# Optimization experiments

Hardware: AMD Instinct MI355X
Metric: run time of the kernel (lower is better)

The kernel has to match this reference:

```python
import jax, jax.numpy as jnp
import numpy as np

B = 2048        # graphs per batch
NC = 81         # cells per sudoku
IN_C, HID = 10, 128
N_ACT, N_NUM, N_TECH = 4, 9, 10


def _sudoku_edges():
    idx = np.arange(NC).reshape(9, 9)
    adj = np.zeros((NC, NC), dtype=bool)
    for i in range(9):
        for j in range(9):
            n = idx[i, j]
            adj[n, idx[i, :]] = True
            adj[n, idx[:, j]] = True
            bi, bj = 3 * (i // 3), 3 * (j // 3)
            adj[n, idx[bi:bi + 3, bj:bj + 3].reshape(-1)] = True
            adj[n, n] = False
    src, dst = np.nonzero(adj)  # 1620 directed edges
    return np.stack([src, dst]).astype(np.int32)


def setup_inputs() -> dict:
    key = jax.random.key(0)
    ks = jax.random.split(key, 12)
    N = B * NC
    base = _sudoku_edges()                          # [2, 1620]
    offs = (np.arange(B, dtype=np.int32) * NC)      # [B]
    ei = (base[:, None, :] + offs[None, :, None]).reshape(2, -1)  # [2, B*1620]
    batch = np.repeat(np.arange(B, dtype=np.int32), NC)           # [N]

    def lin(k, fan_in, fan_out):
        s = 1.0 / np.sqrt(fan_in)
        return jax.random.uniform(k, (fan_in, fan_out), jnp.float32, -s, s)

    return {
        "x": jax.random.normal(ks[0], (N, IN_C), jnp.float32),
        "edge_index": jnp.asarray(ei),
        "batch": jnp.asarray(batch),
        "W1": lin(ks[1], IN_C, HID), "b1": jnp.zeros((HID,), jnp.float32),
        "W2": lin(ks[2], HID, HID),  "b2": jnp.zeros((HID,), jnp.float32),
        "Wa": lin(ks[3], HID, N_ACT),  "ba": jnp.zeros((N_ACT,), jnp.float32),
        "Wc": lin(ks[4], HID, NC),     "bc": jnp.zeros((NC,), jnp.float32),
        "Wn": lin(ks[5], HID, N_NUM),  "bn": jnp.zeros((N_NUM,), jnp.float32),
        "Wt": lin(ks[6], HID, N_TECH), "bt": jnp.zeros((N_TECH,), jnp.float32),
    }


def _gcn_conv(x, edge_index, W, b):
    n = x.shape[0]
    loop = jnp.arange(n, dtype=edge_index.dtype)
    src = jnp.concatenate([edge_index[0], loop])
    dst = jnp.concatenate([edge_index[1], loop])
    deg = jax.ops.segment_sum(jnp.ones_like(dst, jnp.float32), dst, num_segments=n)
    dinv = jax.lax.rsqrt(deg)            # deg >= 1 due to self-loops
    norm = dinv[src] * dinv[dst]         # [E+N]
    h = x @ W                            # [N, out]
    msg = h[src] * norm[:, None]         # gather + scale
    return jax.ops.segment_sum(msg, dst, num_segments=n) + b


def reference(x, edge_index, batch, W1, b1, W2, b2, Wa, ba, Wc, bc, Wn, bn, Wt, bt):
    h = jax.nn.relu(_gcn_conv(x, edge_index, W1, b1))
    h = jax.nn.relu(_gcn_conv(h, edge_index, W2, b2))
    # global mean pool over graphs
    sums = jax.ops.segment_sum(h, batch, num_segments=B)
    cnts = jax.ops.segment_sum(jnp.ones((h.shape[0],), h.dtype), batch, num_segments=B)
    pooled = sums / jnp.maximum(cnts, 1.0)[:, None]   # [B, HID]
    return (pooled @ Wa + ba, pooled @ Wc + bc, pooled @ Wn + bn, pooled @ Wt + bt)
```

## Files before the change

### kernel.cpp

```cpp
#include <hip/hip_runtime.h>
#include <hip/hip_bf16.h>

typedef __attribute__((ext_vector_type(8))) short bf16x8;
typedef __attribute__((ext_vector_type(4))) float f32x4;

__device__ __forceinline__ unsigned short f2b(float f) {
    __hip_bfloat16 h = __float2bfloat16(f);
    return __builtin_bit_cast(unsigned short, h);
}
__device__ __forceinline__ float b2f(unsigned short u) {
    unsigned v = ((unsigned)u) << 16;
    return __builtin_bit_cast(float, v);
}
__device__ __forceinline__ float ldf(const void* p, int idx, bool f32) {
    return f32 ? ((const float*)p)[idx] : b2f(((const unsigned short*)p)[idx]);
}
__device__ __forceinline__ unsigned short ldb(const void* p, int idx, bool f32) {
    return f32 ? f2b(((const float*)p)[idx]) : ((const unsigned short*)p)[idx];
}
__device__ __forceinline__ int swz(int row, int col) {
    return row * 128 + (((col >> 3) ^ (row & 7)) << 3) + (col & 7);
}

__device__ __forceinline__ bool sniff_f32(const void* x) {
    const unsigned* p = (const unsigned*)x;
    int wild = 0;
#pragma unroll
    for (int i = 0; i < 16; ++i) {
        unsigned e = (p[i] >> 7) & 0xFF;
        wild += (e != 0 && (e < 0x68 || e > 0x90)) ? 1 : 0;
    }
    return wild > 8;
}

#define WS_B1F    16
#define WS_B2F    528
#define WS_BHF    1040
#define WS_W1R    1536
#define WS_W2R    9728
#define WS_SR     42496
#define WS_WH     60928

__global__ void k_repack(const void* __restrict__ x,
                         const void* __restrict__ W1, const void* __restrict__ b1,
                         const void* __restrict__ W2, const void* __restrict__ b2,
                         const void* __restrict__ Wa, const void* __restrict__ ba,
                         const void* __restrict__ Wc, const void* __restrict__ bc,
                         const void* __restrict__ Wn, const void* __restrict__ bn,
                         const void* __restrict__ Wt, const void* __restrict__ bt,
                         char* __restrict__ ws) {
    const bool f32 = sniff_f32(x);
    int idx = blockIdx.x * blockDim.x + threadIdx.x;
    if (idx < 4096) {
        int f = idx >> 5, k = idx & 31;
        unsigned short v = (k < 10) ? ldb(W1, k * 128 + f, f32) : (unsigned short)0;
        ((unsigned short*)(ws + WS_W1R))[idx] = v;
        return;
    }
    idx -= 4096;
    if (idx < 16384) {
        int f = idx >> 7, k = idx & 127;
        ((unsigned short*)(ws + WS_W2R))[idx] = ldb(W2, k * 128 + f, f32);
        return;
    }
    idx -= 16384;
    if (idx < 9216) {
        int fi = idx >> 9, rem = idx & 511;
        int lane = rem >> 3, j = rem & 7;
        int mi = fi / 3, kc = fi - mi * 3;
        int node = mi * 16 + (lane & 15);
        int cell = kc * 32 + ((lane >> 4) << 3) + j;
        bool adj = false;
        if (node < 81 && cell < 81) {
            int ni = node / 9, nj = node % 9;
            int ci = cell / 9, cj = cell % 9;
            adj = (ni == ci) || (nj == cj) ||
                  ((ni / 3 == ci / 3) && (nj / 3 == cj / 3));
        }
        ((unsigned short*)(ws + WS_SR))[idx] = adj ? (unsigned short)0x3F80 : (unsigned short)0;
        return;
    }
    idx -= 9216;
    if (idx < 13312) {
        int o = idx >> 7, f = idx & 127;
        const void* W; int oo, dim;
        if (o < 4)       { W = Wa; oo = o;      dim = 4;  }
        else if (o < 85) { W = Wc; oo = o - 4;  dim = 81; }
        else if (o < 94) { W = Wn; oo = o - 85; dim = 9;  }
        else             { W = Wt; oo = o - 94; dim = 10; }
        ((float*)(ws + WS_WH))[idx] = ldf(W, f * dim + oo, f32);
        return;
    }
    idx -= 13312;
    if (idx < 360) {
        float v;
        if (idx < 128)      v = ldf(b1, idx, f32);
        else if (idx < 256) v = ldf(b2, idx - 128, f32);
        else {
            int o = idx - 256;
            if (o < 4)       v = ldf(ba, o, f32);
            else if (o < 85) v = ldf(bc, o - 4, f32);
            else if (o < 94) v = ldf(bn, o - 85, f32);
            else             v = ldf(bt, o - 94, f32);
        }
        if (idx < 128)      ((float*)(ws + WS_B1F))[idx] = v;
        else if (idx < 256) ((float*)(ws + WS_B2F))[idx - 128] = v;
        else                ((float*)(ws + WS_BHF))[idx - 256] = v;
    }
}

__global__ __launch_bounds__(256, 4) void sudoku_gnn(
    const void* __restrict__ x, const char* __restrict__ ws,
    void* __restrict__ out, int nB)
{
    __shared__ __attribute__((aligned(16))) unsigned short sA[16384];
    __shared__ __attribute__((aligned(16))) unsigned int   xs[816];
    __shared__ float sPoolPart[256];
    __shared__ float sPool[128];

    const bool f32 = sniff_f32(x);
    const unsigned short* w1r = (const unsigned short*)(ws + WS_W1R);
    const unsigned short* w2r = (const unsigned short*)(ws + WS_W2R);
    const unsigned short* sr  = (const unsigned short*)(ws + WS_SR);
    const float* b1f = (const float*)(ws + WS_B1F);
    const float* b2f = (const float*)(ws + WS_B2F);
    const float* bhf = (const float*)(ws + WS_BHF);
    const float* whf = (const float*)(ws + WS_WH);

    const int tid  = threadIdx.x;
    const int wave = tid >> 6;
    const int lane = tid & 63;
    const int ln15 = lane & 15;
    const int q    = lane >> 4;
    const int k0   = q * 8;
    const int mtb  = (wave & 1) * 3;
    const int nb   = (wave & 1) * 48;
    const int fb   = (wave >> 1) * 64;
    const int g    = blockIdx.x;
    const float inv21 = 1.0f / 21.0f;

    {
        const int words = f32 ? 810 : 405;
        const unsigned int* src = (const unsigned int*)x + (size_t)g * words;
        for (int i = tid; i < words; i += 256) xs[i] = src[i];
    }

    bf16x8 sfr[3][3];
#pragma unroll
    for (int kc = 0; kc < 3; ++kc)
#pragma unroll
        for (int jt = 0; jt < 3; ++jt)
            sfr[kc][jt] = *(const bf16x8*)&sr[(((mtb + jt) * 3 + kc) * 64 + lane) * 8];
    bf16x8 w1f[4];
#pragma unroll
    for (int nt = 0; nt < 4; ++nt)
        w1f[nt] = *(const bf16x8*)&w1r[(fb + nt * 16 + ln15) * 32 + k0];

    __syncthreads();

    bf16x8 xf[3];
#pragma unroll
    for (int mt = 0; mt < 3; ++mt) {
        int node = (mtb + mt) * 16 + ln15;
        bf16x8 v = {0, 0, 0, 0, 0, 0, 0, 0};
        if (node < 81) {
            int base = node * 10;
            if (q == 0) {
#pragma unroll
                for (int jj = 0; jj < 8; ++jj)
                    v[jj] = (short)(f32 ? f2b(((const float*)xs)[base + jj])
                                        : ((const unsigned short*)xs)[base + jj]);
            } else if (q == 1) {
#pragma unroll
                for (int jj = 0; jj < 2; ++jj)
                    v[jj] = (short)(f32 ? f2b(((const float*)xs)[base + 8 + jj])
                                        : ((const unsigned short*)xs)[base + 8 + jj]);
            }
        }
        xf[mt] = v;
    }

    const f32x4 z4 = {0.f, 0.f, 0.f, 0.f};
    f32x4 acc[3][4];

#pragma unroll
    for (int mt = 0; mt < 3; ++mt)
#pragma unroll
        for (int nt = 0; nt < 4; ++nt)
            acc[mt][nt] = __builtin_amdgcn_mfma_f32_16x16x32_bf16(xf[mt], w1f[nt], z4, 0, 0, 0);
#pragma unroll
    for (int mt = 0; mt < 3; ++mt)
#pragma unroll
        for (int nt = 0; nt < 4; ++nt) {
            int f = fb + nt * 16 + ln15;
            int nodeb = (mtb + mt) * 16 + q * 4;
            unsigned lo = (unsigned)f2b(acc[mt][nt][0]) | ((unsigned)f2b(acc[mt][nt][1]) << 16);
            unsigned hi = (unsigned)f2b(acc[mt][nt][2]) | ((unsigned)f2b(acc[mt][nt][3]) << 16);
            *(uint2*)&sA[swz(f, nodeb)] = make_uint2(lo, hi);
        }
    __syncthreads();

#pragma unroll
    for (int a = 0; a < 3; ++a)
#pragma unroll
        for (int b = 0; b < 4; ++b) acc[a][b] = z4;
#pragma unroll
    for (int kc = 0; kc < 3; ++kc) {
        bf16x8 a4[4];
#pragma unroll
        for (int at = 0; at < 4; ++at)
            a4[at] = *(const bf16x8*)&sA[swz(fb + at * 16 + ln15, kc * 32 + k0)];
#pragma unroll
        for (int at = 0; at < 4; ++at)
#pragma unroll
            for (int jt = 0; jt < 3; ++jt)
                acc[jt][at] = __builtin_amdgcn_mfma_f32_16x16x32_bf16(a4[at], sfr[kc][jt], acc[jt][at], 0, 0, 0);
    }
    __syncthreads();
#pragma unroll
    for (int at = 0; at < 4; ++at) {
        float4 bv = *(const float4*)&b1f[fb + at * 16 + q * 4];
#pragma unroll
        for (int jt = 0; jt < 3; ++jt) {
            int node = nb + jt * 16 + ln15;
            float v0 = fmaxf(acc[jt][at][0] * inv21 + bv.x, 0.0f);
            float v1 = fmaxf(acc[jt][at][1] * inv21 + bv.y, 0.0f);
            float v2 = fmaxf(acc[jt][at][2] * inv21 + bv.z, 0.0f);
            float v3 = fmaxf(acc[jt][at][3] * inv21 + bv.w, 0.0f);
            unsigned lo = (unsigned)f2b(v0) | ((unsigned)f2b(v1) << 16);
            unsigned hi = (unsigned)f2b(v2) | ((unsigned)f2b(v3) << 16);
            *(uint2*)&sA[swz(node, fb + at * 16 + q * 4)] = make_uint2(lo, hi);
        }
    }
    __syncthreads();

#pragma unroll
    for (int a = 0; a < 3; ++a)
#pragma unroll
        for (int b = 0; b < 4; ++b) acc[a][b] = z4;
#pragma unroll
    for (int kc = 0; kc < 4; ++kc) {
        bf16x8 w2f[4];
#pragma unroll
        for (int nt = 0; nt < 4; ++nt)
            w2f[nt] = *(const bf16x8*)&w2r[(fb + nt * 16 + ln15) * 128 + kc * 32 + k0];
        bf16x8 a3[3];
#pragma unroll
        for (int mt = 0; mt < 3; ++mt)
            a3[mt] = *(const bf16x8*)&sA[swz((mtb + mt) * 16 + ln15, kc * 32 + k0)];
#pragma unroll
        for (int mt = 0; mt < 3; ++mt)
#pragma unroll
            for (int nt = 0; nt < 4; ++nt)
                acc[mt][nt] = __builtin_amdgcn_mfma_f32_16x16x32_bf16(a3[mt], w2f[nt], acc[mt][nt], 0, 0, 0);
    }
    __syncthreads();
#pragma unroll
    for (int mt = 0; mt < 3; ++mt)
#pragma unroll
        for (int nt = 0; nt < 4; ++nt) {
            int f = fb + nt * 16 + ln15;
            int nodeb = (mtb + mt) * 16 + q * 4;
            unsigned lo = (unsigned)f2b(acc[mt][nt][0]) | ((unsigned)f2b(acc[mt][nt][1]) << 16);
            unsigned hi = (unsigned)f2b(acc[mt][nt][2]) | ((unsigned)f2b(acc[mt][nt][3]) << 16);
            *(uint2*)&sA[swz(f, nodeb)] = make_uint2(lo, hi);
        }
    __syncthreads();

#pragma unroll
    for (int a = 0; a < 3; ++a)
#pragma unroll
        for (int b = 0; b < 4; ++b) acc[a][b] = z4;
#pragma unroll
    for (int kc = 0; kc < 3; ++kc) {
        bf16x8 a4[4];
#pragma unroll
        for (int at = 0; at < 4; ++at)
            a4[at] = *(const bf16x8*)&sA[swz(fb + at * 16 + ln15, kc * 32 + k0)];
#pragma unroll
        for (int at = 0; at < 4; ++at)
#pragma unroll
            for (int jt = 0; jt < 3; ++jt)
                acc[jt][at] = __builtin_amdgcn_mfma_f32_16x16x32_bf16(a4[at], sfr[kc][jt], acc[jt][at], 0, 0, 0);
    }
#pragma unroll
    for (int at = 0; at < 4; ++at) {
        float4 bv = *(const float4*)&b2f[fb + at * 16 + q * 4];
        float s0 = 0.f, s1 = 0.f, s2 = 0.f, s3 = 0.f;
#pragma unroll
        for (int jt = 0; jt < 3; ++jt) {
            int node = nb + jt * 16 + ln15;
            if (node < 81) {
                s0 += fmaxf(acc[jt][at][0] * inv21 + bv.x, 0.0f);
                s1 += fmaxf(acc[jt][at][1] * inv21 + bv.y, 0.0f);
                s2 += fmaxf(acc[jt][at][2] * inv21 + bv.z, 0.0f);
                s3 += fmaxf(acc[jt][at][3] * inv21 + bv.w, 0.0f);
            }
        }
#pragma unroll
        for (int off = 1; off < 16; off <<= 1) {
            s0 += __shfl_xor(s0, off);
            s1 += __shfl_xor(s1, off);
            s2 += __shfl_xor(s2, off);
            s3 += __shfl_xor(s3, off);
        }
        if (ln15 == 0) {
            float4 v = {s0, s1, s2, s3};
            *(float4*)&sPoolPart[(wave & 1) * 128 + fb + at * 16 + q * 4] = v;
        }
    }
    __syncthreads();
    if (tid < 128) {
        sPool[tid] = (sPoolPart[tid] + sPoolPart[128 + tid]) / 81.0f;
    }
    __syncthreads();

    {
        int o = tid;
        if (o < 104) {
            float a = bhf[o];
            const float4* wrow = (const float4*)(whf + o * 128);
            const float4* sp4  = (const float4*)sPool;
#pragma unroll 8
            for (int i = 0; i < 32; ++i) {
                float4 wv = wrow[i];
                float4 pv = sp4[i];
                a += pv.x * wv.x + pv.y * wv.y + pv.z * wv.z + pv.w * wv.w;
            }
            int oo; size_t off;
            if (o < 4)       { oo = o;      off = (size_t)g * 4 + oo; }
            else if (o < 85) { oo = o - 4;  off = (size_t)nB * 4  + (size_t)g * 81 + oo; }
            else if (o < 94) { oo = o - 85; off = (size_t)nB * 85 + (size_t)g * 9  + oo; }
            else             { oo = o - 94; off = (size_t)nB * 94 + (size_t)g * 10 + oo; }
            if (f32) ((float*)out)[off] = a;
            else     ((unsigned short*)out)[off] = f2b(a);
        }
    }
}

extern "C" void kernel_launch(void* const* d_in, const int* in_sizes, int n_in,
                              void* d_out, int out_size, void* d_ws, size_t ws_size,
                              hipStream_t stream) {
    const void* x  = d_in[0];
    int nB = in_sizes[2] / 81;
    if (nB <= 0) return;

    char* ws = (char*)d_ws;
    hipLaunchKernelGGL(k_repack, dim3(170), dim3(256), 0, stream,
                       x, d_in[3], d_in[4], d_in[5], d_in[6],
                       d_in[7], d_in[8], d_in[9], d_in[10],
                       d_in[11], d_in[12], d_in[13], d_in[14], ws);
    hipLaunchKernelGGL(sudoku_gnn, dim3(nB), dim3(256), 0, stream,
                       x, (const char*)ws, d_out, nB);
}
```

Measured before the change: 145.4 us.

## Process four graphs per block with per-wave feature split and prefetched inputs

Each block now handles four graphs in a loop, and each wave owns 32 output features across all 96 node rows. The structure matrix fragments and weights are loaded into registers once per block and reused across the four graphs. The next graph's input is prefetched into registers, and two shared-memory buffers cut the number of barriers per graph. The cost is higher register pressure (launch bounds lowered to 2 waves per SIMD), more LDS use, and a grid a quarter the size with a serialized per-graph loop.

```diff
diff --git a/kernel.cpp b/kernel.cpp
--- a/kernel.cpp
+++ b/kernel.cpp
@@ -109,14 +109,13 @@
     }
 }
 
-__global__ __launch_bounds__(256, 4) void sudoku_gnn(
+__global__ __launch_bounds__(256, 2) void sudoku_gnn(
     const void* __restrict__ x, const char* __restrict__ ws,
     void* __restrict__ out, int nB)
 {
-    __shared__ __attribute__((aligned(16))) unsigned short sA[16384];
-    __shared__ __attribute__((aligned(16))) unsigned int   xs[816];
-    __shared__ float sPoolPart[256];
-    __shared__ float sPool[128];
+    __shared__ __attribute__((aligned(16))) unsigned short tT[16384];
+    __shared__ __attribute__((aligned(16))) unsigned short hS[12288];
+    __shared__ float sPool[4][128];
 
     const bool f32 = sniff_f32(x);
     const unsigned short* w1r = (const unsigned short*)(ws + WS_W1R);
@@ -133,207 +132,223 @@
     const int ln15 = lane & 15;
     const int q    = lane >> 4;
     const int k0   = q * 8;
-    const int mtb  = (wave & 1) * 3;
-    const int nb   = (wave & 1) * 48;
-    const int fb   = (wave >> 1) * 64;
-    const int g    = blockIdx.x;
+    const int FB   = wave * 32;
+    const int g0   = blockIdx.x * 4;
     const float inv21 = 1.0f / 21.0f;
-
-    {
-        const int words = f32 ? 810 : 405;
-        const unsigned int* src = (const unsigned int*)x + (size_t)g * words;
-        for (int i = tid; i < words; i += 256) xs[i] = src[i];
-    }
-
-    bf16x8 sfr[3][3];
-#pragma unroll
-    for (int kc = 0; kc < 3; ++kc)
-#pragma unroll
-        for (int jt = 0; jt < 3; ++jt)
-            sfr[kc][jt] = *(const bf16x8*)&sr[(((mtb + jt) * 3 + kc) * 64 + lane) * 8];
-    bf16x8 w1f[4];
-#pragma unroll
-    for (int nt = 0; nt < 4; ++nt)
-        w1f[nt] = *(const bf16x8*)&w1r[(fb + nt * 16 + ln15) * 32 + k0];
-
-    __syncthreads();
-
-    bf16x8 xf[3];
-#pragma unroll
-    for (int mt = 0; mt < 3; ++mt) {
-        int node = (mtb + mt) * 16 + ln15;
-        bf16x8 v = {0, 0, 0, 0, 0, 0, 0, 0};
-        if (node < 81) {
-            int base = node * 10;
-            if (q == 0) {
-#pragma unroll
-                for (int jj = 0; jj < 8; ++jj)
-                    v[jj] = (short)(f32 ? f2b(((const float*)xs)[base + jj])
-                                        : ((const unsigned short*)xs)[base + jj]);
-            } else if (q == 1) {
-#pragma unroll
-                for (int jj = 0; jj < 2; ++jj)
-                    v[jj] = (short)(f32 ? f2b(((const float*)xs)[base + 8 + jj])
-                                        : ((const unsigned short*)xs)[base + 8 + jj]);
-            }
-        }
-        xf[mt] = v;
-    }
+    const float inv81 = 1.0f / 81.0f;
+
+    bf16x8 sfr[6][3];
+#pragma unroll
+    for (int nt = 0; nt < 6; ++nt)
+#pragma unroll
+        for (int kc = 0; kc < 3; ++kc)
+            sfr[nt][kc] = *(const bf16x8*)&sr[((nt * 3 + kc) * 64 + lane) * 8];
+    bf16x8 w1f[2];
+#pragma unroll
+    for (int fmt = 0; fmt < 2; ++fmt)
+        w1f[fmt] = *(const bf16x8*)&w1r[(FB + fmt * 16 + ln15) * 32 + k0];
+
+    uint4 pr4[6]; unsigned pr1[6];
+    auto rawload = [&](int g) {
+        const char* xg = (const char*)x + (size_t)(g < nB ? g : nB - 1) * 1620;
+#pragma unroll
+        for (int mt = 0; mt < 6; ++mt) {
+            int node = mt * 16 + ln15;
+            uint4 r = {0, 0, 0, 0}; unsigned r1v = 0;
+            if (node < 81) {
+                if (q == 0)      r   = *(const uint4*)(xg + node * 20);
+                else if (q == 1) r1v = *(const unsigned*)(xg + node * 20 + 16);
+            }
+            pr4[mt] = r; pr1[mt] = r1v;
+        }
+    };
+    if (!f32) rawload(g0);
 
     const f32x4 z4 = {0.f, 0.f, 0.f, 0.f};
-    f32x4 acc[3][4];
-
-#pragma unroll
-    for (int mt = 0; mt < 3; ++mt)
-#pragma unroll
-        for (int nt = 0; nt < 4; ++nt)
-            acc[mt][nt] = __builtin_amdgcn_mfma_f32_16x16x32_bf16(xf[mt], w1f[nt], z4, 0, 0, 0);
-#pragma unroll
-    for (int mt = 0; mt < 3; ++mt)
-#pragma unroll
-        for (int nt = 0; nt < 4; ++nt) {
-            int f = fb + nt * 16 + ln15;
-            int nodeb = (mtb + mt) * 16 + q * 4;
-            unsigned lo = (unsigned)f2b(acc[mt][nt][0]) | ((unsigned)f2b(acc[mt][nt][1]) << 16);
-            unsigned hi = (unsigned)f2b(acc[mt][nt][2]) | ((unsigned)f2b(acc[mt][nt][3]) << 16);
-            *(uint2*)&sA[swz(f, nodeb)] = make_uint2(lo, hi);
-        }
-    __syncthreads();
-
-#pragma unroll
-    for (int a = 0; a < 3; ++a)
-#pragma unroll
-        for (int b = 0; b < 4; ++b) acc[a][b] = z4;
-#pragma unroll
-    for (int kc = 0; kc < 3; ++kc) {
-        bf16x8 a4[4];
-#pragma unroll
-        for (int at = 0; at < 4; ++at)
-            a4[at] = *(const bf16x8*)&sA[swz(fb + at * 16 + ln15, kc * 32 + k0)];
-#pragma unroll
-        for (int at = 0; at < 4; ++at)
-#pragma unroll
-            for (int jt = 0; jt < 3; ++jt)
-                acc[jt][at] = __builtin_amdgcn_mfma_f32_16x16x32_bf16(a4[at], sfr[kc][jt], acc[jt][at], 0, 0, 0);
-    }
-    __syncthreads();
-#pragma unroll
-    for (int at = 0; at < 4; ++at) {
-        float4 bv = *(const float4*)&b1f[fb + at * 16 + q * 4];
-#pragma unroll
-        for (int jt = 0; jt < 3; ++jt) {
-            int node = nb + jt * 16 + ln15;
-            float v0 = fmaxf(acc[jt][at][0] * inv21 + bv.x, 0.0f);
-            float v1 = fmaxf(acc[jt][at][1] * inv21 + bv.y, 0.0f);
-            float v2 = fmaxf(acc[jt][at][2] * inv21 + bv.z, 0.0f);
-            float v3 = fmaxf(acc[jt][at][3] * inv21 + bv.w, 0.0f);
-            unsigned lo = (unsigned)f2b(v0) | ((unsigned)f2b(v1) << 16);
-            unsigned hi = (unsigned)f2b(v2) | ((unsigned)f2b(v3) << 16);
-            *(uint2*)&sA[swz(node, fb + at * 16 + q * 4)] = make_uint2(lo, hi);
-        }
-    }
-    __syncthreads();
-
-#pragma unroll
-    for (int a = 0; a < 3; ++a)
-#pragma unroll
-        for (int b = 0; b < 4; ++b) acc[a][b] = z4;
-#pragma unroll
-    for (int kc = 0; kc < 4; ++kc) {
-        bf16x8 w2f[4];
-#pragma unroll
-        for (int nt = 0; nt < 4; ++nt)
-            w2f[nt] = *(const bf16x8*)&w2r[(fb + nt * 16 + ln15) * 128 + kc * 32 + k0];
-        bf16x8 a3[3];
-#pragma unroll
-        for (int mt = 0; mt < 3; ++mt)
-            a3[mt] = *(const bf16x8*)&sA[swz((mtb + mt) * 16 + ln15, kc * 32 + k0)];
-#pragma unroll
-        for (int mt = 0; mt < 3; ++mt)
-#pragma unroll
-            for (int nt = 0; nt < 4; ++nt)
-                acc[mt][nt] = __builtin_amdgcn_mfma_f32_16x16x32_bf16(a3[mt], w2f[nt], acc[mt][nt], 0, 0, 0);
-    }
-    __syncthreads();
-#pragma unroll
-    for (int mt = 0; mt < 3; ++mt)
-#pragma unroll
-        for (int nt = 0; nt < 4; ++nt) {
-            int f = fb + nt * 16 + ln15;
-            int nodeb = (mtb + mt) * 16 + q * 4;
-            unsigned lo = (unsigned)f2b(acc[mt][nt][0]) | ((unsigned)f2b(acc[mt][nt][1]) << 16);
-            unsigned hi = (unsigned)f2b(acc[mt][nt][2]) | ((unsigned)f2b(acc[mt][nt][3]) << 16);
-            *(uint2*)&sA[swz(f, nodeb)] = make_uint2(lo, hi);
-        }
-    __syncthreads();
-
-#pragma unroll
-    for (int a = 0; a < 3; ++a)
-#pragma unroll
-        for (int b = 0; b < 4; ++b) acc[a][b] = z4;
-#pragma unroll
-    for (int kc = 0; kc < 3; ++kc) {
-        bf16x8 a4[4];
-#pragma unroll
-        for (int at = 0; at < 4; ++at)
-            a4[at] = *(const bf16x8*)&sA[swz(fb + at * 16 + ln15, kc * 32 + k0)];
-#pragma unroll
-        for (int at = 0; at < 4; ++at)
-#pragma unroll
-            for (int jt = 0; jt < 3; ++jt)
-                acc[jt][at] = __builtin_amdgcn_mfma_f32_16x16x32_bf16(a4[at], sfr[kc][jt], acc[jt][at], 0, 0, 0);
-    }
-#pragma unroll
-    for (int at = 0; at < 4; ++at) {
-        float4 bv = *(const float4*)&b2f[fb + at * 16 + q * 4];
-        float s0 = 0.f, s1 = 0.f, s2 = 0.f, s3 = 0.f;
-#pragma unroll
-        for (int jt = 0; jt < 3; ++jt) {
-            int node = nb + jt * 16 + ln15;
-            if (node < 81) {
-                s0 += fmaxf(acc[jt][at][0] * inv21 + bv.x, 0.0f);
-                s1 += fmaxf(acc[jt][at][1] * inv21 + bv.y, 0.0f);
-                s2 += fmaxf(acc[jt][at][2] * inv21 + bv.z, 0.0f);
-                s3 += fmaxf(acc[jt][at][3] * inv21 + bv.w, 0.0f);
-            }
-        }
-#pragma unroll
-        for (int off = 1; off < 16; off <<= 1) {
-            s0 += __shfl_xor(s0, off);
-            s1 += __shfl_xor(s1, off);
-            s2 += __shfl_xor(s2, off);
-            s3 += __shfl_xor(s3, off);
-        }
-        if (ln15 == 0) {
-            float4 v = {s0, s1, s2, s3};
-            *(float4*)&sPoolPart[(wave & 1) * 128 + fb + at * 16 + q * 4] = v;
-        }
-    }
-    __syncthreads();
-    if (tid < 128) {
-        sPool[tid] = (sPoolPart[tid] + sPoolPart[128 + tid]) / 81.0f;
-    }
-    __syncthreads();
-
-    {
-        int o = tid;
-        if (o < 104) {
-            float a = bhf[o];
-            const float4* wrow = (const float4*)(whf + o * 128);
-            const float4* sp4  = (const float4*)sPool;
+
+    for (int gi = 0; gi < 4; ++gi) {
+        const int g = g0 + gi;
+
+        bf16x8 xf[6];
+        if (!f32) {
+#pragma unroll
+            for (int mt = 0; mt < 6; ++mt) {
+                bf16x8 v = {0, 0, 0, 0, 0, 0, 0, 0};
+                if (q == 0)      v = __builtin_bit_cast(bf16x8, pr4[mt]);
+                else if (q == 1) { v[0] = (short)(pr1[mt] & 0xFFFF); v[1] = (short)(pr1[mt] >> 16); }
+                xf[mt] = v;
+            }
+            if (gi < 3) rawload(g + 1);
+        } else {
+            const float* xg = (const float*)x + (size_t)(g < nB ? g : nB - 1) * 810;
+#pragma unroll
+            for (int mt = 0; mt < 6; ++mt) {
+                int node = mt * 16 + ln15;
+                bf16x8 v = {0, 0, 0, 0, 0, 0, 0, 0};
+                if (node < 81) {
+                    if (q == 0) {
+#pragma unroll
+                        for (int j = 0; j < 8; ++j) v[j] = (short)f2b(xg[node * 10 + j]);
+                    } else if (q == 1) {
+                        v[0] = (short)f2b(xg[node * 10 + 8]);
+                        v[1] = (short)f2b(xg[node * 10 + 9]);
+                    }
+                }
+                xf[mt] = v;
+            }
+        }
+
+#pragma unroll
+        for (int fmt = 0; fmt < 2; ++fmt)
+#pragma unroll
+            for (int mt = 0; mt < 6; ++mt) {
+                f32x4 c = __builtin_amdgcn_mfma_f32_16x16x32_bf16(xf[mt], w1f[fmt], z4, 0, 0, 0);
+                unsigned lo = (unsigned)f2b(c[0]) | ((unsigned)f2b(c[1]) << 16);
+                unsigned hi = (unsigned)f2b(c[2]) | ((unsigned)f2b(c[3]) << 16);
+                *(uint2*)&tT[swz(FB + fmt * 16 + ln15, mt * 16 + q * 4)] = make_uint2(lo, hi);
+            }
+
+        f32x4 acc[2][6];
+#pragma unroll
+        for (int a = 0; a < 2; ++a)
+#pragma unroll
+            for (int b = 0; b < 6; ++b) acc[a][b] = z4;
+#pragma unroll
+        for (int kc = 0; kc < 3; ++kc) {
+            bf16x8 af[2];
+#pragma unroll
+            for (int fmt = 0; fmt < 2; ++fmt)
+                af[fmt] = *(const bf16x8*)&tT[swz(FB + fmt * 16 + ln15, kc * 32 + k0)];
+#pragma unroll
+            for (int fmt = 0; fmt < 2; ++fmt)
+#pragma unroll
+                for (int nt = 0; nt < 6; ++nt)
+                    acc[fmt][nt] = __builtin_amdgcn_mfma_f32_16x16x32_bf16(af[fmt], sfr[nt][kc], acc[fmt][nt], 0, 0, 0);
+        }
+#pragma unroll
+        for (int fmt = 0; fmt < 2; ++fmt) {
+            float4 bv = *(const float4*)&b1f[FB + fmt * 16 + q * 4];
+#pragma unroll
+            for (int nt = 0; nt < 6; ++nt) {
+                float v0 = fmaxf(acc[fmt][nt][0] * inv21 + bv.x, 0.0f);
+                float v1 = fmaxf(acc[fmt][nt][1] * inv21 + bv.y, 0.0f);
+                float v2 = fmaxf(acc[fmt][nt][2] * inv21 + bv.z, 0.0f);
+                float v3 = fmaxf(acc[fmt][nt][3] * inv21 + bv.w, 0.0f);
+                unsigned lo = (unsigned)f2b(v0) | ((unsigned)f2b(v1) << 16);
+                unsigned hi = (unsigned)f2b(v2) | ((unsigned)f2b(v3) << 16);
+                *(uint2*)&hS[swz(nt * 16 + ln15, FB + fmt * 16 + q * 4)] = make_uint2(lo, hi);
+            }
+        }
+        __syncthreads();
+
+        f32x4 acc3[6][2];
+#pragma unroll
+        for (int a = 0; a < 6; ++a)
+#pragma unroll
+            for (int b = 0; b < 2; ++b) acc3[a][b] = z4;
+        bf16x8 wB[2];
+#pragma unroll
+        for (int fmt = 0; fmt < 2; ++fmt)
+            wB[fmt] = *(const bf16x8*)&w2r[(FB + fmt * 16 + ln15) * 128 + k0];
+#pragma unroll
+        for (int kc = 0; kc < 4; ++kc) {
+            bf16x8 wN[2];
+            if (kc < 3) {
+#pragma unroll
+                for (int fmt = 0; fmt < 2; ++fmt)
+                    wN[fmt] = *(const bf16x8*)&w2r[(FB + fmt * 16 + ln15) * 128 + (kc + 1) * 32 + k0];
+            }
+            bf16x8 a3[6];
+#pragma unroll
+            for (int mt = 0; mt < 6; ++mt)
+                a3[mt] = *(const bf16x8*)&hS[swz(mt * 16 + ln15, kc * 32 + k0)];
+#pragma unroll
+            for (int mt = 0; mt < 6; ++mt)
+#pragma unroll
+                for (int fmt = 0; fmt < 2; ++fmt)
+                    acc3[mt][fmt] = __builtin_amdgcn_mfma_f32_16x16x32_bf16(a3[mt], wB[fmt], acc3[mt][fmt], 0, 0, 0);
+            if (kc < 3) { wB[0] = wN[0]; wB[1] = wN[1]; }
+        }
+#pragma unroll
+        for (int mt = 0; mt < 6; ++mt)
+#pragma unroll
+            for (int fmt = 0; fmt < 2; ++fmt) {
+                unsigned lo = (unsigned)f2b(acc3[mt][fmt][0]) | ((unsigned)f2b(acc3[mt][fmt][1]) << 16);
+                unsigned hi = (unsigned)f2b(acc3[mt][fmt][2]) | ((unsigned)f2b(acc3[mt][fmt][3]) << 16);
+                *(uint2*)&tT[swz(FB + fmt * 16 + ln15, mt * 16 + q * 4)] = make_uint2(lo, hi);
+            }
+
+        f32x4 acc4[2][6];
+#pragma unroll
+        for (int a = 0; a < 2; ++a)
+#pragma unroll
+            for (int b = 0; b < 6; ++b) acc4[a][b] = z4;
+#pragma unroll
+        for (int kc = 0; kc < 3; ++kc) {
+            bf16x8 af[2];
+#pragma unroll
+            for (int fmt = 0; fmt < 2; ++fmt)
+                af[fmt] = *(const bf16x8*)&tT[swz(FB + fmt * 16 + ln15, kc * 32 + k0)];
+#pragma unroll
+            for (int fmt = 0; fmt < 2; ++fmt)
+#pragma unroll
+                for (int nt = 0; nt < 6; ++nt)
+                    acc4[fmt][nt] = __builtin_amdgcn_mfma_f32_16x16x32_bf16(af[fmt], sfr[nt][kc], acc4[fmt][nt], 0, 0, 0);
+        }
+#pragma unroll
+        for (int fmt = 0; fmt < 2; ++fmt) {
+            float4 bv = *(const float4*)&b2f[FB + fmt * 16 + q * 4];
+            float s0 = 0.f, s1 = 0.f, s2 = 0.f, s3 = 0.f;
+#pragma unroll
+            for (int nt = 0; nt < 6; ++nt) {
+                int node = nt * 16 + ln15;
+                if (node < 81) {
+                    s0 += fmaxf(acc4[fmt][nt][0] * inv21 + bv.x, 0.0f);
+                    s1 += fmaxf(acc4[fmt][nt][1] * inv21 + bv.y, 0.0f);
+                    s2 += fmaxf(acc4[fmt][nt][2] * inv21 + bv.z, 0.0f);
+                    s3 += fmaxf(acc4[fmt][nt][3] * inv21 + bv.w, 0.0f);
+                }
+            }
+#pragma unroll
+            for (int off = 1; off < 16; off <<= 1) {
+                s0 += __shfl_xor(s0, off);
+                s1 += __shfl_xor(s1, off);
+                s2 += __shfl_xor(s2, off);
+                s3 += __shfl_xor(s3, off);
+            }
+            if (ln15 == 0) {
+                float4 v = {s0 * inv81, s1 * inv81, s2 * inv81, s3 * inv81};
+                *(float4*)&sPool[gi][FB + fmt * 16 + q * 4] = v;
+            }
+        }
+        __syncthreads();
+    }
+
+#pragma unroll
+    for (int it = 0; it < 2; ++it) {
+        int item = tid + it * 256;
+        if (item < 416) {
+            int gi = item / 104;
+            int o  = item - gi * 104;
+            int g  = g0 + gi;
+            if (g < nB) {
+                float a = bhf[o];
+                const float4* wrow = (const float4*)(whf + o * 128);
+                const float4* sp4  = (const float4*)sPool[gi];
 #pragma unroll 8
-            for (int i = 0; i < 32; ++i) {
-                float4 wv = wrow[i];
-                float4 pv = sp4[i];
-                a += pv.x * wv.x + pv.y * wv.y + pv.z * wv.z + pv.w * wv.w;
-            }
-            int oo; size_t off;
-            if (o < 4)       { oo = o;      off = (size_t)g * 4 + oo; }
-            else if (o < 85) { oo = o - 4;  off = (size_t)nB * 4  + (size_t)g * 81 + oo; }
-            else if (o < 94) { oo = o - 85; off = (size_t)nB * 85 + (size_t)g * 9  + oo; }
-            else             { oo = o - 94; off = (size_t)nB * 94 + (size_t)g * 10 + oo; }
-            if (f32) ((float*)out)[off] = a;
-            else     ((unsigned short*)out)[off] = f2b(a);
+                for (int i = 0; i < 32; ++i) {
+                    float4 wv = wrow[i];
+                    float4 pv = sp4[i];
+                    a += pv.x * wv.x + pv.y * wv.y + pv.z * wv.z + pv.w * wv.w;
+                }
+                int oo; size_t off;
+                if (o < 4)       { oo = o;      off = (size_t)g * 4 + oo; }
+                else if (o < 85) { oo = o - 4;  off = (size_t)nB * 4  + (size_t)g * 81 + oo; }
+                else if (o < 94) { oo = o - 85; off = (size_t)nB * 85 + (size_t)g * 9  + oo; }
+                else             { oo = o - 94; off = (size_t)nB * 94 + (size_t)g * 10 + oo; }
+                if (f32) ((float*)out)[off] = a;
+                else     ((unsigned short*)out)[off] = f2b(a);
+            }
         }
     }
 }
@@ -350,6 +365,6 @@
                        x, d_in[3], d_in[4], d_in[5], d_in[6],
                        d_in[7], d_in[8], d_in[9], d_in[10],
                        d_in[11], d_in[12], d_in[13], d_in[14], ws);
-    hipLaunchKernelGGL(sudoku_gnn, dim3(nB), dim3(256), 0, stream,
+    hipLaunchKernelGGL(sudoku_gnn, dim3((nB + 3) / 4), dim3(256), 0, stream,
                        x, (const char*)ws, d_out, nB);
 }
```

Measured after the change: 152.6 us. 5.0% more time.
